# Optimization experiments

Hardware: AMD Instinct MI355X
Metric: run time of the kernel (lower is better)

The kernel has to match this reference:

```python
import jax, jax.numpy as jnp
import numpy as np

B, L, S, E, D = 16, 2048, 2048, 64, 64

def setup_inputs() -> dict:
    key = jax.random.key(0)
    k1, k2, k3, k4 = jax.random.split(key, 4)
    queries = jax.random.normal(k1, (B, L, E), dtype=jnp.float32)
    keys = jax.random.normal(k2, (B, S, E), dtype=jnp.float32)
    values = jax.random.normal(k3, (B, S, D), dtype=jnp.float32)
    mlp = jax.random.normal(k4, (L, L), dtype=jnp.float32)  # learned seq-mix matrix
    return {"queries": queries, "keys": keys, "values": values, "mlp": mlp}

def reference(queries, keys, values, mlp):
    # scale = 1/sqrt(E) (self.scale is None)
    E_dim = queries.shape[-1]
    scale = 1.0 / jnp.sqrt(jnp.asarray(E_dim, dtype=queries.dtype))
    # scores: [B, L, S]
    scores = jnp.einsum('ble,bse->bls', queries, keys)
    # dropout omitted (eval mode / attention_dropout=0)
    A = jax.nn.softmax(scale * scores, axis=-1)
    # attention output: [B, L, D]
    V = jnp.einsum('bls,bsd->bld', A, values)
    # learned sequence-mixing: [B, L, D] -> [B, P, D] with P == L
    out = jnp.einsum('bld,pl->bpd', V, mlp)
    return out
```

## Files before the change

kernel.cpp:

```cpp
#include <hip/hip_runtime.h>

#define NB 16
#define NL 2048
#define NS 2048
#define NE 64
#define ND 64

typedef float floatx4 __attribute__((ext_vector_type(4)));
typedef _Float16 half8 __attribute__((ext_vector_type(8)));
typedef __fp16 half2v __attribute__((ext_vector_type(2)));

union H8 { half8 v; half2v h2[4]; };

__device__ __forceinline__ half8 cvt8(floatx4 a, floatx4 b) {
  H8 h;
  h.h2[0] = __builtin_amdgcn_cvt_pkrtz(a[0], a[1]);
  h.h2[1] = __builtin_amdgcn_cvt_pkrtz(a[2], a[3]);
  h.h2[2] = __builtin_amdgcn_cvt_pkrtz(b[0], b[1]);
  h.h2[3] = __builtin_amdgcn_cvt_pkrtz(b[2], b[3]);
  return h.v;
}

__device__ __forceinline__ void async16(void* l, const void* g) {
  __builtin_amdgcn_global_load_lds((__attribute__((address_space(1))) void*)g,
                                   (__attribute__((address_space(3))) void*)l, 16, 0, 0);
}

__device__ __forceinline__ int kinv(int y) {
  return (y & 0x23) | ((y & 8) << 1) | ((y & 4) << 1) | ((y & 16) >> 2);
}

__global__ __launch_bounds__(256) void prep_k(const float* __restrict__ V,
                                              const float* __restrict__ K,
                                              const float* __restrict__ M,
                                              _Float16* __restrict__ Vt,
                                              _Float16* __restrict__ Kh,
                                              _Float16* __restrict__ Mh,
                                              int do_km) {
  __shared__ __align__(16) _Float16 Vl[64][72];
  const int bid = blockIdx.x;
  const int t = threadIdx.x;

  if (bid < 512) {
    const int b = bid >> 5;
    const int s0 = (bid & 31) * 64;
    {
      int sl = t & 63;
      int dg = t >> 6;
      const float* src = V + ((size_t)(b * NS + s0 + sl)) * ND + dg * 16;
      int x = kinv(sl);
      #pragma unroll
      for (int c = 0; c < 4; ++c) {
        floatx4 v = *(const floatx4*)(src + c * 4);
        #pragma unroll
        for (int e = 0; e < 4; ++e) Vl[dg * 16 + c * 4 + e][x] = (_Float16)v[e];
      }
    }
    __syncthreads();
    {
      int d = t & 63;
      int xg = t >> 6;
      int dk = (d & 7) << 3;
      #pragma unroll
      for (int h = 0; h < 2; ++h) {
        int x = xg * 16 + h * 8;
        half8 v = *(const half8*)&Vl[d][x];
        *(half8*)(Vt + ((size_t)(b * ND + d)) * NS + s0 + (x ^ dk)) = v;
      }
    }
  } else if (bid < 1536) {
    if (!do_km) return;
    int c = (bid - 512) * 256 + t;
    int j = c & 7;
    int s = (c >> 3) & (NS - 1);
    int b = c >> 14;
    const float* src = K + ((size_t)(b * NS + s)) * NE + j * 8;
    half8 h = cvt8(*(const floatx4*)src, *(const floatx4*)(src + 4));
    *(half8*)(Kh + ((size_t)(b * NS + s)) * NE + (j ^ (s & 7)) * 8) = h;
  } else {
    if (!do_km) return;
    int c = (bid - 1536) * 256 + t;
    int j = c & 255;
    int p = c >> 8;
    const float* src = M + (size_t)p * NL + j * 8;
    half8 h = cvt8(*(const floatx4*)src, *(const floatx4*)(src + 4));
    int jo = (j & ~7) | ((j & 7) ^ (p & 7));
    *(half8*)(Mh + (size_t)p * NL + jo * 8) = h;
  }
}

template<bool KH16>
__global__ __launch_bounds__(256) void attn_k(const float* __restrict__ Q,
                                              const void* __restrict__ Ksrc,
                                              const _Float16* __restrict__ Vtp,
                                              _Float16* __restrict__ Vatt) {
  __shared__ __align__(16) char smem[32768];
  const int tid = threadIdx.x;
  const int wid = tid >> 6, lane = tid & 63;
  const int lr = lane & 15, lg = lane >> 4;
  const int g = wid & 1;
  const int qh = wid >> 1;
  const int b = blockIdx.y;
  const int qbase = blockIdx.x * 64 + qh * 32;
  const _Float16* Kh = (const _Float16*)Ksrc;
  const float* Kf = (const float*)Ksrc;

  constexpr float SC = 0.18033688f;
  half8 qf[2][2];
  #pragma unroll
  for (int sub = 0; sub < 2; ++sub)
    #pragma unroll
    for (int kk = 0; kk < 2; ++kk) {
      const float* qp = Q + ((size_t)(b * NL + qbase + sub * 16 + lr)) * NE + kk * 32 + lg * 8;
      floatx4 a = *(const floatx4*)qp, c = *(const floatx4*)(qp + 4);
      qf[sub][kk] = cvt8(a * SC, c * SC);
    }

  floatx4 oacc[2][4];
  #pragma unroll
  for (int s = 0; s < 2; ++s)
    #pragma unroll
    for (int m = 0; m < 4; ++m) oacc[s][m] = (floatx4){0.f, 0.f, 0.f, 0.f};
  float lrun[2] = {0.f, 0.f};

  auto stageV = [&](int buf, int s0) {
    #pragma unroll
    for (int i = 0; i < 2; ++i) {
      int co = (wid * 2 + i) * 1024;
      int o = co + lane * 16;
      int row = o >> 7, c8 = (o >> 4) & 7;
      async16(smem + 16384 + buf * 8192 + co,
              Vtp + ((size_t)(b * ND + row)) * NS + s0 + c8 * 8);
    }
  };
  auto stageK = [&](int buf, int s0) {
    if constexpr (KH16) {
      #pragma unroll
      for (int i = 0; i < 2; ++i) {
        int co = (wid * 2 + i) * 1024;
        int o = co + lane * 16;
        int row = o >> 7, c8 = (o >> 4) & 7;
        async16(smem + buf * 8192 + co,
                Kh + ((size_t)(b * NS + s0 + row)) * NE + c8 * 8);
      }
    } else {
      int row = tid >> 2, cg = (tid & 3) * 16;
      const float* kp = Kf + ((size_t)(b * NS + s0 + row)) * NE + cg;
      #pragma unroll
      for (int c = 0; c < 2; ++c) {
        half8 h = cvt8(*(const floatx4*)(kp + c * 8), *(const floatx4*)(kp + c * 8 + 4));
        int col = cg + c * 8;
        *(half8*)(smem + buf * 8192 + ((row * 128 + col * 2) ^ ((row & 7) << 4))) = h;
      }
    }
  };

  stageK(0, 0); stageV(0, 0);
  __syncthreads();

  for (int t = 0; t < NS / 64; ++t) {
    int buf = t & 1;
    if (t + 1 < NS / 64) { stageK(buf ^ 1, (t + 1) * 64); stageV(buf ^ 1, (t + 1) * 64); }

    const char* kb = smem + buf * 8192;
    const char* vb = smem + 16384 + buf * 8192;

    half8 kf[2][2];
    #pragma unroll
    for (int mt = 0; mt < 2; ++mt)
      #pragma unroll
      for (int kk = 0; kk < 2; ++kk) {
        int row = g * 32 + mt * 16 + lr, col = kk * 32 + lg * 8;
        kf[mt][kk] = *(const half8*)(kb + ((row * 128 + col * 2) ^ ((row & 7) << 4)));
      }

    H8 bf[2];
    #pragma unroll
    for (int sub = 0; sub < 2; ++sub) {
      floatx4 sacc[2];
      #pragma unroll
      for (int mt = 0; mt < 2; ++mt) sacc[mt] = (floatx4){0.f, 0.f, 0.f, 0.f};
      __builtin_amdgcn_s_setprio(1);
      #pragma unroll
      for (int kk = 0; kk < 2; ++kk)
        #pragma unroll
        for (int mt = 0; mt < 2; ++mt)
          sacc[mt] = __builtin_amdgcn_mfma_f32_16x16x32_f16(kf[mt][kk], qf[sub][kk], sacc[mt], 0, 0, 0);
      __builtin_amdgcn_s_setprio(0);

      float lloc = 0.f;
      half2v w[2][2];
      #pragma unroll
      for (int mt = 0; mt < 2; ++mt) {
        float p0 = __builtin_amdgcn_exp2f(sacc[mt][0]);
        float p1 = __builtin_amdgcn_exp2f(sacc[mt][1]);
        float p2 = __builtin_amdgcn_exp2f(sacc[mt][2]);
        float p3 = __builtin_amdgcn_exp2f(sacc[mt][3]);
        lloc += (p0 + p1) + (p2 + p3);
        w[mt][0] = __builtin_amdgcn_cvt_pkrtz(p0, p1);
        w[mt][1] = __builtin_amdgcn_cvt_pkrtz(p2, p3);
      }
      lloc += __shfl_xor(lloc, 16, 64);
      lloc += __shfl_xor(lloc, 32, 64);
      lrun[sub] += lloc;
      bf[sub].h2[0] = w[0][0];
      bf[sub].h2[1] = w[0][1];
      bf[sub].h2[2] = w[1][0];
      bf[sub].h2[3] = w[1][1];
    }

    __builtin_amdgcn_s_setprio(1);
    #pragma unroll
    for (int mt = 0; mt < 4; ++mt) {
      int row = mt * 16 + lr, col = g * 32 + lg * 8;
      half8 vt = *(const half8*)(vb + ((row * 128 + col * 2) ^ ((row & 7) << 4)));
      oacc[0][mt] = __builtin_amdgcn_mfma_f32_16x16x32_f16(vt, bf[0].v, oacc[0][mt], 0, 0, 0);
      oacc[1][mt] = __builtin_amdgcn_mfma_f32_16x16x32_f16(vt, bf[1].v, oacc[1][mt], 0, 0, 0);
    }
    __builtin_amdgcn_s_setprio(0);
    __syncthreads();
  }

  {
    char* red = smem + qh * 16384;
    if (g == 1) {
      #pragma unroll
      for (int sub = 0; sub < 2; ++sub)
        #pragma unroll
        for (int mt = 0; mt < 4; ++mt)
          *(floatx4*)(red + lane * 144 + (sub * 4 + mt) * 16) = oacc[sub][mt];
      if (lg == 0) {
        *(float*)(red + 9216 + lr * 8) = lrun[0];
        *(float*)(red + 9216 + lr * 8 + 4) = lrun[1];
      }
    }
    __syncthreads();
    if (g == 0) {
      #pragma unroll
      for (int sub = 0; sub < 2; ++sub) {
        float lt = lrun[sub] + *(const float*)(red + 9216 + lr * 8 + sub * 4);
        float inv = __builtin_amdgcn_rcpf(lt);
        int l = qbase + sub * 16 + lr;
        #pragma unroll
        for (int mt = 0; mt < 4; ++mt) {
          floatx4 o = oacc[sub][mt] + *(const floatx4*)(red + lane * 144 + (sub * 4 + mt) * 16);
          #pragma unroll
          for (int r = 0; r < 4; ++r) {
            int d = mt * 16 + lg * 4 + r;
            int lsw = (l & ~63) | ((l & 63) ^ ((d & 7) << 3));
            Vatt[((size_t)(b * ND + d)) * NL + lsw] = (_Float16)(o[r] * inv);
          }
        }
      }
    }
  }
}

template<bool A16>
__global__ __launch_bounds__(256) void mix_k(const void* __restrict__ Asrc,
                                             const _Float16* __restrict__ Bsrc,
                                             float* __restrict__ out) {
  __shared__ __align__(16) char smem[65536];
  const int tid = threadIdx.x;
  const int wid = tid >> 6, lane = tid & 63;
  const int lr = lane & 15, lg = lane >> 4;
  const int kh = wid & 1;
  const int mw = wid >> 1;
  const int p0 = blockIdx.x * 64;
  const int b = blockIdx.y;
  const _Float16* Ah = (const _Float16*)Asrc;
  const float* Af = (const float*)Asrc;

  floatx4 acc[2][4];
  #pragma unroll
  for (int mt = 0; mt < 2; ++mt)
    #pragma unroll
    for (int nt = 0; nt < 4; ++nt) acc[mt][nt] = (floatx4){0.f, 0.f, 0.f, 0.f};

  auto stage = [&](int buf, int t) {
    int k0 = kh * (NL / 2) + t * 64;
    if constexpr (A16) {
      #pragma unroll
      for (int i = 0; i < 4; ++i) {
        int co = (mw * 4 + i) * 1024;
        int o = co + lane * 16;
        int row = o >> 7, c8 = (o >> 4) & 7;
        async16(smem + kh * 16384 + buf * 8192 + co,
                Ah + ((size_t)(p0 + row)) * NL + k0 + c8 * 8);
      }
    } else {
      int row = (lane & 31) + mw * 32, cg = (lane >> 5) * 32;
      const float* ap = Af + ((size_t)(p0 + row)) * NL + k0 + cg;
      #pragma unroll
      for (int c = 0; c < 4; ++c) {
        half8 h = cvt8(*(const floatx4*)(ap + c * 8), *(const floatx4*)(ap + c * 8 + 4));
        int col = cg + c * 8;
        *(half8*)(smem + kh * 16384 + buf * 8192 +
                  ((row * 128 + col * 2) ^ ((row & 7) << 4))) = h;
      }
    }
    #pragma unroll
    for (int i = 0; i < 4; ++i) {
      int co = (mw * 4 + i) * 1024;
      int o = co + lane * 16;
      int row = o >> 7, c8 = (o >> 4) & 7;
      async16(smem + 32768 + kh * 16384 + buf * 8192 + co,
              Bsrc + ((size_t)(b * ND + row)) * NL + k0 + c8 * 8);
    }
  };

  stage(0, 0);
  __syncthreads();

  for (int t = 0; t < 16; ++t) {
    int buf = t & 1;
    if (t + 1 < 16) stage(buf ^ 1, t + 1);
    const char* ab = smem + kh * 16384 + buf * 8192;
    const char* bb = smem + 32768 + kh * 16384 + buf * 8192;
    #pragma unroll
    for (int kk = 0; kk < 2; ++kk) {
      int col = kk * 32 + lg * 8;
      half8 af[2];
      #pragma unroll
      for (int mt = 0; mt < 2; ++mt) {
        int row = mw * 32 + mt * 16 + lr;
        af[mt] = *(const half8*)(ab + ((row * 128 + col * 2) ^ ((row & 7) << 4)));
      }
      __builtin_amdgcn_s_setprio(1);
      #pragma unroll
      for (int nt = 0; nt < 4; ++nt) {
        int row = nt * 16 + lr;
        half8 bfr = *(const half8*)(bb + ((row * 128 + col * 2) ^ ((row & 7) << 4)));
        #pragma unroll
        for (int mt = 0; mt < 2; ++mt)
          acc[mt][nt] = __builtin_amdgcn_mfma_f32_16x16x32_f16(af[mt], bfr, acc[mt][nt], 0, 0, 0);
      }
      __builtin_amdgcn_s_setprio(0);
    }
    __syncthreads();
  }

  if (kh == 1) {
    #pragma unroll
    for (int mt = 0; mt < 2; ++mt)
      #pragma unroll
      for (int nt = 0; nt < 4; ++nt) {
        int idx = mt * 4 + nt;
        *(floatx4*)(smem + mw * 8192 + lane * 128 + ((idx ^ (lane & 7)) * 16)) = acc[mt][nt];
      }
  }
  __syncthreads();
  if (kh == 0) {
    #pragma unroll
    for (int mt = 0; mt < 2; ++mt)
      #pragma unroll
      for (int nt = 0; nt < 4; ++nt) {
        int idx = mt * 4 + nt;
        acc[mt][nt] += *(const floatx4*)(smem + mw * 8192 + lane * 128 + ((idx ^ (lane & 7)) * 16));
        #pragma unroll
        for (int r = 0; r < 4; ++r) {
          int p = p0 + mw * 32 + mt * 16 + lg * 4 + r;
          int d = nt * 16 + lr;
          out[((size_t)(b * NL + p)) * ND + d] = acc[mt][nt][r];
        }
      }
  }
}

extern "C" void kernel_launch(void* const* d_in, const int* in_sizes, int n_in,
                              void* d_out, int out_size, void* d_ws, size_t ws_size,
                              hipStream_t stream) {
  (void)in_sizes; (void)n_in; (void)out_size;
  const float* Q = (const float*)d_in[0];
  const float* K = (const float*)d_in[1];
  const float* V = (const float*)d_in[2];
  const float* M = (const float*)d_in[3];
  float* out = (float*)d_out;

  char* ws = (char*)d_ws;
  _Float16* Vtp  = (_Float16*)ws;
  _Float16* Vatt = (_Float16*)(ws + (4u << 20));
  _Float16* Kh   = (_Float16*)(ws + (8u << 20));
  _Float16* Mh   = (_Float16*)(ws + (12u << 20));
  bool big = ws_size >= (size_t)(20u << 20);

  if (big) {
    prep_k<<<3584, 256, 0, stream>>>(V, K, M, Vtp, Kh, Mh, 1);
    attn_k<true><<<dim3(32, 16), 256, 0, stream>>>(Q, Kh, Vtp, Vatt);
    mix_k<true><<<dim3(32, 16), 256, 0, stream>>>(Mh, Vatt, out);
  } else {
    prep_k<<<512, 256, 0, stream>>>(V, K, M, Vtp, Kh, Mh, 0);
    attn_k<false><<<dim3(32, 16), 256, 0, stream>>>(Q, K, Vtp, Vatt);
    mix_k<false><<<dim3(32, 16), 256, 0, stream>>>(M, Vatt, out);
  }
}
```

Measured before the change: 60.02 us.

## Double attention key tile to 128 and move mlp fp16 conversion into attention tail

The attention loop now processes 128 keys per iteration instead of 64, doubling the LDS staging buffers to 64KB and halving the number of barriers and loop iterations. The fp32-to-fp16 conversion of the mixing matrix moves out of the prep kernel and into the tail of the attention kernel, so the prep launch is smaller. The larger LDS footprint may reduce how many blocks fit per CU, and each attention block gains extra tail work.

```diff
diff --git a/kernel.cpp b/kernel.cpp
--- a/kernel.cpp
+++ b/kernel.cpp
@@ -32,11 +32,9 @@
 
 __global__ __launch_bounds__(256) void prep_k(const float* __restrict__ V,
                                               const float* __restrict__ K,
-                                              const float* __restrict__ M,
                                               _Float16* __restrict__ Vt,
                                               _Float16* __restrict__ Kh,
-                                              _Float16* __restrict__ Mh,
-                                              int do_km) {
+                                              int do_k) {
   __shared__ __align__(16) _Float16 Vl[64][72];
   const int bid = blockIdx.x;
   const int t = threadIdx.x;
@@ -68,8 +66,8 @@
         *(half8*)(Vt + ((size_t)(b * ND + d)) * NS + s0 + (x ^ dk)) = v;
       }
     }
-  } else if (bid < 1536) {
-    if (!do_km) return;
+  } else {
+    if (!do_k) return;
     int c = (bid - 512) * 256 + t;
     int j = c & 7;
     int s = (c >> 3) & (NS - 1);
@@ -77,15 +75,6 @@
     const float* src = K + ((size_t)(b * NS + s)) * NE + j * 8;
     half8 h = cvt8(*(const floatx4*)src, *(const floatx4*)(src + 4));
     *(half8*)(Kh + ((size_t)(b * NS + s)) * NE + (j ^ (s & 7)) * 8) = h;
-  } else {
-    if (!do_km) return;
-    int c = (bid - 1536) * 256 + t;
-    int j = c & 255;
-    int p = c >> 8;
-    const float* src = M + (size_t)p * NL + j * 8;
-    half8 h = cvt8(*(const floatx4*)src, *(const floatx4*)(src + 4));
-    int jo = (j & ~7) | ((j & 7) ^ (p & 7));
-    *(half8*)(Mh + (size_t)p * NL + jo * 8) = h;
   }
 }
 
@@ -93,8 +82,10 @@
 __global__ __launch_bounds__(256) void attn_k(const float* __restrict__ Q,
                                               const void* __restrict__ Ksrc,
                                               const _Float16* __restrict__ Vtp,
-                                              _Float16* __restrict__ Vatt) {
-  __shared__ __align__(16) char smem[32768];
+                                              _Float16* __restrict__ Vatt,
+                                              const float* __restrict__ Mf,
+                                              _Float16* __restrict__ Mh) {
+  __shared__ __align__(16) char smem[65536];
   const int tid = threadIdx.x;
   const int wid = tid >> 6, lane = tid & 63;
   const int lr = lane & 15, lg = lane >> 4;
@@ -125,32 +116,32 @@
 
   auto stageV = [&](int buf, int s0) {
     #pragma unroll
-    for (int i = 0; i < 2; ++i) {
-      int co = (wid * 2 + i) * 1024;
+    for (int i = 0; i < 4; ++i) {
+      int co = (wid * 4 + i) * 1024;
       int o = co + lane * 16;
-      int row = o >> 7, c8 = (o >> 4) & 7;
-      async16(smem + 16384 + buf * 8192 + co,
-              Vtp + ((size_t)(b * ND + row)) * NS + s0 + c8 * 8);
+      int row = o >> 8, c16 = (o >> 4) & 15;
+      async16(smem + 32768 + buf * 16384 + co,
+              Vtp + ((size_t)(b * ND + row)) * NS + s0 + c16 * 8);
     }
   };
   auto stageK = [&](int buf, int s0) {
     if constexpr (KH16) {
       #pragma unroll
-      for (int i = 0; i < 2; ++i) {
-        int co = (wid * 2 + i) * 1024;
+      for (int i = 0; i < 4; ++i) {
+        int co = (wid * 4 + i) * 1024;
         int o = co + lane * 16;
         int row = o >> 7, c8 = (o >> 4) & 7;
-        async16(smem + buf * 8192 + co,
+        async16(smem + buf * 16384 + co,
                 Kh + ((size_t)(b * NS + s0 + row)) * NE + c8 * 8);
       }
     } else {
-      int row = tid >> 2, cg = (tid & 3) * 16;
+      int row = tid >> 1, cg = (tid & 1) * 32;
       const float* kp = Kf + ((size_t)(b * NS + s0 + row)) * NE + cg;
       #pragma unroll
-      for (int c = 0; c < 2; ++c) {
+      for (int c = 0; c < 4; ++c) {
         half8 h = cvt8(*(const floatx4*)(kp + c * 8), *(const floatx4*)(kp + c * 8 + 4));
         int col = cg + c * 8;
-        *(half8*)(smem + buf * 8192 + ((row * 128 + col * 2) ^ ((row & 7) << 4))) = h;
+        *(half8*)(smem + buf * 16384 + ((row * 128 + col * 2) ^ ((row & 7) << 4))) = h;
       }
     }
   };
@@ -158,40 +149,40 @@
   stageK(0, 0); stageV(0, 0);
   __syncthreads();
 
-  for (int t = 0; t < NS / 64; ++t) {
+  for (int t = 0; t < NS / 128; ++t) {
     int buf = t & 1;
-    if (t + 1 < NS / 64) { stageK(buf ^ 1, (t + 1) * 64); stageV(buf ^ 1, (t + 1) * 64); }
-
-    const char* kb = smem + buf * 8192;
-    const char* vb = smem + 16384 + buf * 8192;
-
-    half8 kf[2][2];
-    #pragma unroll
-    for (int mt = 0; mt < 2; ++mt)
+    if (t + 1 < NS / 128) { stageK(buf ^ 1, (t + 1) * 128); stageV(buf ^ 1, (t + 1) * 128); }
+
+    const char* kb = smem + buf * 16384;
+    const char* vb = smem + 32768 + buf * 16384;
+
+    half8 kf[4][2];
+    #pragma unroll
+    for (int mt = 0; mt < 4; ++mt)
       #pragma unroll
       for (int kk = 0; kk < 2; ++kk) {
-        int row = g * 32 + mt * 16 + lr, col = kk * 32 + lg * 8;
+        int row = g * 64 + mt * 16 + lr, col = kk * 32 + lg * 8;
         kf[mt][kk] = *(const half8*)(kb + ((row * 128 + col * 2) ^ ((row & 7) << 4)));
       }
 
-    H8 bf[2];
+    H8 bf[2][2];
     #pragma unroll
     for (int sub = 0; sub < 2; ++sub) {
-      floatx4 sacc[2];
-      #pragma unroll
-      for (int mt = 0; mt < 2; ++mt) sacc[mt] = (floatx4){0.f, 0.f, 0.f, 0.f};
+      floatx4 sacc[4];
+      #pragma unroll
+      for (int mt = 0; mt < 4; ++mt) sacc[mt] = (floatx4){0.f, 0.f, 0.f, 0.f};
       __builtin_amdgcn_s_setprio(1);
       #pragma unroll
       for (int kk = 0; kk < 2; ++kk)
         #pragma unroll
-        for (int mt = 0; mt < 2; ++mt)
+        for (int mt = 0; mt < 4; ++mt)
           sacc[mt] = __builtin_amdgcn_mfma_f32_16x16x32_f16(kf[mt][kk], qf[sub][kk], sacc[mt], 0, 0, 0);
       __builtin_amdgcn_s_setprio(0);
 
       float lloc = 0.f;
-      half2v w[2][2];
-      #pragma unroll
-      for (int mt = 0; mt < 2; ++mt) {
+      half2v w[4][2];
+      #pragma unroll
+      for (int mt = 0; mt < 4; ++mt) {
         float p0 = __builtin_amdgcn_exp2f(sacc[mt][0]);
         float p1 = __builtin_amdgcn_exp2f(sacc[mt][1]);
         float p2 = __builtin_amdgcn_exp2f(sacc[mt][2]);
@@ -203,20 +194,26 @@
       lloc += __shfl_xor(lloc, 16, 64);
       lloc += __shfl_xor(lloc, 32, 64);
       lrun[sub] += lloc;
-      bf[sub].h2[0] = w[0][0];
-      bf[sub].h2[1] = w[0][1];
-      bf[sub].h2[2] = w[1][0];
-      bf[sub].h2[3] = w[1][1];
+      #pragma unroll
+      for (int kk = 0; kk < 2; ++kk) {
+        bf[sub][kk].h2[0] = w[2 * kk][0];
+        bf[sub][kk].h2[1] = w[2 * kk][1];
+        bf[sub][kk].h2[2] = w[2 * kk + 1][0];
+        bf[sub][kk].h2[3] = w[2 * kk + 1][1];
+      }
     }
 
     __builtin_amdgcn_s_setprio(1);
     #pragma unroll
-    for (int mt = 0; mt < 4; ++mt) {
-      int row = mt * 16 + lr, col = g * 32 + lg * 8;
-      half8 vt = *(const half8*)(vb + ((row * 128 + col * 2) ^ ((row & 7) << 4)));
-      oacc[0][mt] = __builtin_amdgcn_mfma_f32_16x16x32_f16(vt, bf[0].v, oacc[0][mt], 0, 0, 0);
-      oacc[1][mt] = __builtin_amdgcn_mfma_f32_16x16x32_f16(vt, bf[1].v, oacc[1][mt], 0, 0, 0);
-    }
+    for (int kk = 0; kk < 2; ++kk)
+      #pragma unroll
+      for (int mt = 0; mt < 4; ++mt) {
+        int row = mt * 16 + lr;
+        int off = ((kk * 32 + lg * 8) * 2) ^ ((row & 7) << 4);
+        half8 vt = *(const half8*)(vb + row * 256 + g * 128 + off);
+        oacc[0][mt] = __builtin_amdgcn_mfma_f32_16x16x32_f16(vt, bf[0][kk].v, oacc[0][mt], 0, 0, 0);
+        oacc[1][mt] = __builtin_amdgcn_mfma_f32_16x16x32_f16(vt, bf[1][kk].v, oacc[1][mt], 0, 0, 0);
+      }
     __builtin_amdgcn_s_setprio(0);
     __syncthreads();
   }
@@ -252,6 +249,19 @@
           }
         }
       }
+    }
+  }
+
+  if constexpr (KH16) {
+    int mb = blockIdx.y * 32 + blockIdx.x;
+    #pragma unroll
+    for (int q = 0; q < 4; ++q) {
+      int c = mb * 1024 + q * 256 + tid;
+      int j = c & 255, p = c >> 8;
+      const float* src = Mf + (size_t)p * NL + j * 8;
+      half8 h = cvt8(*(const floatx4*)src, *(const floatx4*)(src + 4));
+      int jo = (j & ~7) | ((j & 7) ^ (p & 7));
+      *(half8*)(Mh + (size_t)p * NL + jo * 8) = h;
     }
   }
 }
@@ -385,12 +395,12 @@
   bool big = ws_size >= (size_t)(20u << 20);
 
   if (big) {
-    prep_k<<<3584, 256, 0, stream>>>(V, K, M, Vtp, Kh, Mh, 1);
-    attn_k<true><<<dim3(32, 16), 256, 0, stream>>>(Q, Kh, Vtp, Vatt);
+    prep_k<<<1536, 256, 0, stream>>>(V, K, Vtp, Kh, 1);
+    attn_k<true><<<dim3(32, 16), 256, 0, stream>>>(Q, Kh, Vtp, Vatt, M, Mh);
     mix_k<true><<<dim3(32, 16), 256, 0, stream>>>(Mh, Vatt, out);
   } else {
-    prep_k<<<512, 256, 0, stream>>>(V, K, M, Vtp, Kh, Mh, 0);
-    attn_k<false><<<dim3(32, 16), 256, 0, stream>>>(Q, K, Vtp, Vatt);
+    prep_k<<<512, 256, 0, stream>>>(V, K, Vtp, Kh, 0);
+    attn_k<false><<<dim3(32, 16), 256, 0, stream>>>(Q, K, Vtp, Vatt, nullptr, nullptr);
     mix_k<false><<<dim3(32, 16), 256, 0, stream>>>(M, Vatt, out);
   }
 }
```

New measurement: 56.09 us. -6.6%, faster.

## Halve attention query tile, move M conversion into attention tail, relax barriers

Applied to the files above, without the earlier changes.

The attention kernel now handles 16 query rows per wave instead of 32, which doubles the grid to 1024 blocks so more work can be in flight. The fp16 conversion of the mixing matrix moves out of the prep kernel into the tail of the attention kernel, shortening prep. In the fp16 paths, full __syncthreads are replaced by explicit vmcnt/lgkmcnt waits plus s_barrier, so the next tile's async loads can remain outstanding across the barrier. The trade-off is that each K/V tile loaded into LDS is reused by half as many queries, and correctness now depends on the hand-set wait counts.

```diff
diff --git a/kernel.cpp b/kernel.cpp
--- a/kernel.cpp
+++ b/kernel.cpp
@@ -26,17 +26,20 @@
                                    (__attribute__((address_space(3))) void*)l, 16, 0, 0);
 }
 
+#define B1_WAIT4  { asm volatile("s_waitcnt vmcnt(4)" ::: "memory"); __builtin_amdgcn_s_barrier(); }
+#define B1_WAIT8  { asm volatile("s_waitcnt vmcnt(8)" ::: "memory"); __builtin_amdgcn_s_barrier(); }
+#define B1_WAIT0  { asm volatile("s_waitcnt vmcnt(0)" ::: "memory"); __builtin_amdgcn_s_barrier(); }
+#define B2_LGKM   { asm volatile("s_waitcnt lgkmcnt(0)" ::: "memory"); __builtin_amdgcn_s_barrier(); }
+
 __device__ __forceinline__ int kinv(int y) {
   return (y & 0x23) | ((y & 8) << 1) | ((y & 4) << 1) | ((y & 16) >> 2);
 }
 
 __global__ __launch_bounds__(256) void prep_k(const float* __restrict__ V,
                                               const float* __restrict__ K,
-                                              const float* __restrict__ M,
                                               _Float16* __restrict__ Vt,
                                               _Float16* __restrict__ Kh,
-                                              _Float16* __restrict__ Mh,
-                                              int do_km) {
+                                              int do_k) {
   __shared__ __align__(16) _Float16 Vl[64][72];
   const int bid = blockIdx.x;
   const int t = threadIdx.x;
@@ -68,8 +71,8 @@
         *(half8*)(Vt + ((size_t)(b * ND + d)) * NS + s0 + (x ^ dk)) = v;
       }
     }
-  } else if (bid < 1536) {
-    if (!do_km) return;
+  } else {
+    if (!do_k) return;
     int c = (bid - 512) * 256 + t;
     int j = c & 7;
     int s = (c >> 3) & (NS - 1);
@@ -77,15 +80,6 @@
     const float* src = K + ((size_t)(b * NS + s)) * NE + j * 8;
     half8 h = cvt8(*(const floatx4*)src, *(const floatx4*)(src + 4));
     *(half8*)(Kh + ((size_t)(b * NS + s)) * NE + (j ^ (s & 7)) * 8) = h;
-  } else {
-    if (!do_km) return;
-    int c = (bid - 1536) * 256 + t;
-    int j = c & 255;
-    int p = c >> 8;
-    const float* src = M + (size_t)p * NL + j * 8;
-    half8 h = cvt8(*(const floatx4*)src, *(const floatx4*)(src + 4));
-    int jo = (j & ~7) | ((j & 7) ^ (p & 7));
-    *(half8*)(Mh + (size_t)p * NL + jo * 8) = h;
   }
 }
 
@@ -93,7 +87,9 @@
 __global__ __launch_bounds__(256) void attn_k(const float* __restrict__ Q,
                                               const void* __restrict__ Ksrc,
                                               const _Float16* __restrict__ Vtp,
-                                              _Float16* __restrict__ Vatt) {
+                                              _Float16* __restrict__ Vatt,
+                                              const float* __restrict__ Mf,
+                                              _Float16* __restrict__ Mh) {
   __shared__ __align__(16) char smem[32768];
   const int tid = threadIdx.x;
   const int wid = tid >> 6, lane = tid & 63;
@@ -101,27 +97,23 @@
   const int g = wid & 1;
   const int qh = wid >> 1;
   const int b = blockIdx.y;
-  const int qbase = blockIdx.x * 64 + qh * 32;
+  const int qbase = blockIdx.x * 32 + qh * 16;
   const _Float16* Kh = (const _Float16*)Ksrc;
   const float* Kf = (const float*)Ksrc;
 
   constexpr float SC = 0.18033688f;
-  half8 qf[2][2];
+  half8 qf[2];
   #pragma unroll
-  for (int sub = 0; sub < 2; ++sub)
-    #pragma unroll
-    for (int kk = 0; kk < 2; ++kk) {
-      const float* qp = Q + ((size_t)(b * NL + qbase + sub * 16 + lr)) * NE + kk * 32 + lg * 8;
-      floatx4 a = *(const floatx4*)qp, c = *(const floatx4*)(qp + 4);
-      qf[sub][kk] = cvt8(a * SC, c * SC);
-    }
-
-  floatx4 oacc[2][4];
+  for (int kk = 0; kk < 2; ++kk) {
+    const float* qp = Q + ((size_t)(b * NL + qbase + lr)) * NE + kk * 32 + lg * 8;
+    floatx4 a = *(const floatx4*)qp, c = *(const floatx4*)(qp + 4);
+    qf[kk] = cvt8(a * SC, c * SC);
+  }
+
+  floatx4 oacc[4];
   #pragma unroll
-  for (int s = 0; s < 2; ++s)
-    #pragma unroll
-    for (int m = 0; m < 4; ++m) oacc[s][m] = (floatx4){0.f, 0.f, 0.f, 0.f};
-  float lrun[2] = {0.f, 0.f};
+  for (int m = 0; m < 4; ++m) oacc[m] = (floatx4){0.f, 0.f, 0.f, 0.f};
+  float lrun = 0.f;
 
   auto stageV = [&](int buf, int s0) {
     #pragma unroll
@@ -156,11 +148,16 @@
   };
 
   stageK(0, 0); stageV(0, 0);
-  __syncthreads();
+  if constexpr (!KH16) __syncthreads();
 
   for (int t = 0; t < NS / 64; ++t) {
     int buf = t & 1;
-    if (t + 1 < NS / 64) { stageK(buf ^ 1, (t + 1) * 64); stageV(buf ^ 1, (t + 1) * 64); }
+    if (t + 1 < NS / 64) {
+      stageK(buf ^ 1, (t + 1) * 64); stageV(buf ^ 1, (t + 1) * 64);
+      if constexpr (KH16) B1_WAIT4 else __syncthreads();
+    } else {
+      if constexpr (KH16) B1_WAIT0
+    }
 
     const char* kb = smem + buf * 8192;
     const char* vb = smem + 16384 + buf * 8192;
@@ -174,84 +171,86 @@
         kf[mt][kk] = *(const half8*)(kb + ((row * 128 + col * 2) ^ ((row & 7) << 4)));
       }
 
-    H8 bf[2];
-    #pragma unroll
-    for (int sub = 0; sub < 2; ++sub) {
-      floatx4 sacc[2];
-      #pragma unroll
-      for (int mt = 0; mt < 2; ++mt) sacc[mt] = (floatx4){0.f, 0.f, 0.f, 0.f};
-      __builtin_amdgcn_s_setprio(1);
-      #pragma unroll
-      for (int kk = 0; kk < 2; ++kk)
-        #pragma unroll
-        for (int mt = 0; mt < 2; ++mt)
-          sacc[mt] = __builtin_amdgcn_mfma_f32_16x16x32_f16(kf[mt][kk], qf[sub][kk], sacc[mt], 0, 0, 0);
-      __builtin_amdgcn_s_setprio(0);
-
-      float lloc = 0.f;
-      half2v w[2][2];
-      #pragma unroll
-      for (int mt = 0; mt < 2; ++mt) {
-        float p0 = __builtin_amdgcn_exp2f(sacc[mt][0]);
-        float p1 = __builtin_amdgcn_exp2f(sacc[mt][1]);
-        float p2 = __builtin_amdgcn_exp2f(sacc[mt][2]);
-        float p3 = __builtin_amdgcn_exp2f(sacc[mt][3]);
-        lloc += (p0 + p1) + (p2 + p3);
-        w[mt][0] = __builtin_amdgcn_cvt_pkrtz(p0, p1);
-        w[mt][1] = __builtin_amdgcn_cvt_pkrtz(p2, p3);
-      }
-      lloc += __shfl_xor(lloc, 16, 64);
-      lloc += __shfl_xor(lloc, 32, 64);
-      lrun[sub] += lloc;
-      bf[sub].h2[0] = w[0][0];
-      bf[sub].h2[1] = w[0][1];
-      bf[sub].h2[2] = w[1][0];
-      bf[sub].h2[3] = w[1][1];
-    }
-
+    floatx4 sacc[2];
+    #pragma unroll
+    for (int mt = 0; mt < 2; ++mt) sacc[mt] = (floatx4){0.f, 0.f, 0.f, 0.f};
     __builtin_amdgcn_s_setprio(1);
     #pragma unroll
+    for (int kk = 0; kk < 2; ++kk)
+      #pragma unroll
+      for (int mt = 0; mt < 2; ++mt)
+        sacc[mt] = __builtin_amdgcn_mfma_f32_16x16x32_f16(kf[mt][kk], qf[kk], sacc[mt], 0, 0, 0);
+    __builtin_amdgcn_s_setprio(0);
+
+    float lloc = 0.f;
+    half2v w[2][2];
+    #pragma unroll
+    for (int mt = 0; mt < 2; ++mt) {
+      float p0 = __builtin_amdgcn_exp2f(sacc[mt][0]);
+      float p1 = __builtin_amdgcn_exp2f(sacc[mt][1]);
+      float p2 = __builtin_amdgcn_exp2f(sacc[mt][2]);
+      float p3 = __builtin_amdgcn_exp2f(sacc[mt][3]);
+      lloc += (p0 + p1) + (p2 + p3);
+      w[mt][0] = __builtin_amdgcn_cvt_pkrtz(p0, p1);
+      w[mt][1] = __builtin_amdgcn_cvt_pkrtz(p2, p3);
+    }
+    lloc += __shfl_xor(lloc, 16, 64);
+    lloc += __shfl_xor(lloc, 32, 64);
+    lrun += lloc;
+    H8 bf;
+    bf.h2[0] = w[0][0];
+    bf.h2[1] = w[0][1];
+    bf.h2[2] = w[1][0];
+    bf.h2[3] = w[1][1];
+
+    __builtin_amdgcn_s_setprio(1);
+    #pragma unroll
     for (int mt = 0; mt < 4; ++mt) {
-      int row = mt * 16 + lr, col = g * 32 + lg * 8;
-      half8 vt = *(const half8*)(vb + ((row * 128 + col * 2) ^ ((row & 7) << 4)));
-      oacc[0][mt] = __builtin_amdgcn_mfma_f32_16x16x32_f16(vt, bf[0].v, oacc[0][mt], 0, 0, 0);
-      oacc[1][mt] = __builtin_amdgcn_mfma_f32_16x16x32_f16(vt, bf[1].v, oacc[1][mt], 0, 0, 0);
+      int row = mt * 16 + lr;
+      int off = ((g * 32 + lg * 8) * 2) ^ ((row & 7) << 4);
+      half8 vt = *(const half8*)(vb + row * 128 + off);
+      oacc[mt] = __builtin_amdgcn_mfma_f32_16x16x32_f16(vt, bf.v, oacc[mt], 0, 0, 0);
     }
     __builtin_amdgcn_s_setprio(0);
-    __syncthreads();
+    if constexpr (KH16) B2_LGKM else __syncthreads();
   }
 
   {
-    char* red = smem + qh * 16384;
+    char* red = smem + qh * 8192;
     if (g == 1) {
       #pragma unroll
-      for (int sub = 0; sub < 2; ++sub)
-        #pragma unroll
-        for (int mt = 0; mt < 4; ++mt)
-          *(floatx4*)(red + lane * 144 + (sub * 4 + mt) * 16) = oacc[sub][mt];
-      if (lg == 0) {
-        *(float*)(red + 9216 + lr * 8) = lrun[0];
-        *(float*)(red + 9216 + lr * 8 + 4) = lrun[1];
-      }
+      for (int mt = 0; mt < 4; ++mt)
+        *(floatx4*)(red + mt * 1024 + lane * 16) = oacc[mt];
+      if (lg == 0) *(float*)(red + 4096 + lr * 4) = lrun;
     }
     __syncthreads();
     if (g == 0) {
-      #pragma unroll
-      for (int sub = 0; sub < 2; ++sub) {
-        float lt = lrun[sub] + *(const float*)(red + 9216 + lr * 8 + sub * 4);
-        float inv = __builtin_amdgcn_rcpf(lt);
-        int l = qbase + sub * 16 + lr;
+      float lt = lrun + *(const float*)(red + 4096 + lr * 4);
+      float inv = __builtin_amdgcn_rcpf(lt);
+      int l = qbase + lr;
+      #pragma unroll
+      for (int mt = 0; mt < 4; ++mt) {
+        floatx4 o = oacc[mt] + *(const floatx4*)(red + mt * 1024 + lane * 16);
         #pragma unroll
-        for (int mt = 0; mt < 4; ++mt) {
-          floatx4 o = oacc[sub][mt] + *(const floatx4*)(red + lane * 144 + (sub * 4 + mt) * 16);
-          #pragma unroll
-          for (int r = 0; r < 4; ++r) {
-            int d = mt * 16 + lg * 4 + r;
-            int lsw = (l & ~63) | ((l & 63) ^ ((d & 7) << 3));
-            Vatt[((size_t)(b * ND + d)) * NL + lsw] = (_Float16)(o[r] * inv);
-          }
+        for (int r = 0; r < 4; ++r) {
+          int d = mt * 16 + lg * 4 + r;
+          int lsw = (l & ~63) | ((l & 63) ^ ((d & 7) << 3));
+          Vatt[((size_t)(b * ND + d)) * NL + lsw] = (_Float16)(o[r] * inv);
         }
       }
+    }
+  }
+
+  if constexpr (KH16) {
+    int mb = blockIdx.y * 64 + blockIdx.x;
+    #pragma unroll
+    for (int q = 0; q < 2; ++q) {
+      int c = mb * 512 + q * 256 + tid;
+      int j = c & 255, p = c >> 8;
+      const float* src = Mf + (size_t)p * NL + j * 8;
+      half8 h = cvt8(*(const floatx4*)src, *(const floatx4*)(src + 4));
+      int jo = (j & ~7) | ((j & 7) ^ (p & 7));
+      *(half8*)(Mh + (size_t)p * NL + jo * 8) = h;
     }
   }
 }
@@ -310,11 +309,16 @@
   };
 
   stage(0, 0);
-  __syncthreads();
+  if constexpr (!A16) __syncthreads();
 
   for (int t = 0; t < 16; ++t) {
     int buf = t & 1;
-    if (t + 1 < 16) stage(buf ^ 1, t + 1);
+    if (t + 1 < 16) {
+      stage(buf ^ 1, t + 1);
+      if constexpr (A16) B1_WAIT8 else __syncthreads();
+    } else {
+      if constexpr (A16) B1_WAIT0
+    }
     const char* ab = smem + kh * 16384 + buf * 8192;
     const char* bb = smem + 32768 + kh * 16384 + buf * 8192;
     #pragma unroll
@@ -337,7 +341,7 @@
       }
       __builtin_amdgcn_s_setprio(0);
     }
-    __syncthreads();
+    if constexpr (A16) B2_LGKM else __syncthreads();
   }
 
   if (kh == 1) {
@@ -385,12 +389,12 @@
   bool big = ws_size >= (size_t)(20u << 20);
 
   if (big) {
-    prep_k<<<3584, 256, 0, stream>>>(V, K, M, Vtp, Kh, Mh, 1);
-    attn_k<true><<<dim3(32, 16), 256, 0, stream>>>(Q, Kh, Vtp, Vatt);
+    prep_k<<<1536, 256, 0, stream>>>(V, K, Vtp, Kh, 1);
+    attn_k<true><<<dim3(64, 16), 256, 0, stream>>>(Q, Kh, Vtp, Vatt, M, Mh);
     mix_k<true><<<dim3(32, 16), 256, 0, stream>>>(Mh, Vatt, out);
   } else {
-    prep_k<<<512, 256, 0, stream>>>(V, K, M, Vtp, Kh, Mh, 0);
-    attn_k<false><<<dim3(32, 16), 256, 0, stream>>>(Q, K, Vtp, Vatt);
+    prep_k<<<512, 256, 0, stream>>>(V, K, Vtp, Kh, 0);
+    attn_k<false><<<dim3(64, 16), 256, 0, stream>>>(Q, K, Vtp, Vatt, nullptr, nullptr);
     mix_k<false><<<dim3(32, 16), 256, 0, stream>>>(M, Vatt, out);
   }
 }
```

After: 64.88 us. 1.08x slower.
